# Kernel optimization log

Measured on AMD Instinct MI355X. Metric: run time of the kernel, lower is better.

Reference implementation:

```python
import jax, jax.numpy as jnp
import numpy as np

N_QUBITS = 8
DEPTH = 1
INPUT_DIM = 64
HIDDEN = 8  # must equal N_QUBITS
SEQ = 64
BATCH = 256


def _apply_rx(state, wire, ang):
    # state: (B, 2, 2, ..., 2) with wire w on axis 1+w; ang: (B,) angles
    n = state.ndim - 1
    st = jnp.moveaxis(state, 1 + wire, -1)
    a0, a1 = st[..., 0], st[..., 1]
    half = ang * 0.5
    c = jnp.cos(half).reshape((-1,) + (1,) * (n - 1))
    s = jnp.sin(half).reshape((-1,) + (1,) * (n - 1))
    new = jnp.stack([c * a0 - 1j * s * a1, c * a1 - 1j * s * a0], axis=-1)
    return jnp.moveaxis(new, -1, 1 + wire)


def _apply_cnot(state, cw, tw):
    st = jnp.moveaxis(state, (1 + cw, 1 + tw), (-2, -1))
    st = st.at[..., 1, :].set(st[..., 1, ::-1])  # flip target where control=1
    return jnp.moveaxis(st, (-2, -1), (1 + cw, 1 + tw))


def qgate(theta, qparams):
    # theta: (B, n) data-dependent RX angles; qparams: (n,) trainable RX angles
    B, n = theta.shape
    state = jnp.zeros((B,) + (2,) * n, dtype=jnp.complex64)
    state = state.at[(slice(None),) + (0,) * n].set(1.0 + 0.0j)  # |0...0>
    for w in range(n):
        state = _apply_rx(state, w, theta[:, w])
    for w in range(n - 1):
        state = _apply_cnot(state, w, w + 1)
    for w in range(n):
        state = _apply_rx(state, w, jnp.broadcast_to(qparams[w], (B,)))
    probs = jnp.abs(state) ** 2  # (B, 2, ..., 2)
    expz = []
    for w in range(n):
        pw = probs.sum(axis=tuple(a for a in range(1, n + 1) if a != 1 + w))  # (B, 2)
        expz.append(pw[:, 0] - pw[:, 1])  # <Z_w>
    return jnp.stack(expz, axis=1)  # (B, n)


def setup_inputs() -> dict:
    key = jax.random.key(0)
    ks = jax.random.split(key, 13)
    d_in = INPUT_DIM + HIDDEN
    d_out = N_QUBITS * DEPTH
    sc = 1.0 / np.sqrt(d_in)
    inp = {"inputs": jax.random.normal(ks[0], (SEQ, BATCH, INPUT_DIM), dtype=jnp.float32)}
    names = ["f", "i", "g", "o"]
    for j, nm in enumerate(names):
        inp["W" + nm] = jax.random.uniform(ks[1 + 3 * j], (d_out, d_in), minval=-sc, maxval=sc, dtype=jnp.float32)
        inp["b" + nm] = jax.random.uniform(ks[2 + 3 * j], (d_out,), minval=-sc, maxval=sc, dtype=jnp.float32)
        inp["q" + nm] = jax.random.normal(ks[3 + 3 * j], (d_out,), dtype=jnp.float32)
    return inp


def reference(inputs, Wf, bf, qf, Wi, bi, qi, Wg, bg, qg, Wo, bo, qo):
    B = inputs.shape[1]
    hx0 = jnp.zeros((B, HIDDEN), dtype=inputs.dtype)
    cx0 = jnp.zeros((B, HIDDEN), dtype=inputs.dtype)

    def step(carry, x_t):
        hx, cx = carry
        comb = jnp.concatenate([x_t, hx], axis=1)  # (B, input+hidden)
        f = jax.nn.sigmoid(qgate(comb @ Wf.T + bf, qf))
        i_ = jax.nn.sigmoid(qgate(comb @ Wi.T + bi, qi))
        g = jnp.tanh(qgate(comb @ Wg.T + bg, qg))
        o = jax.nn.sigmoid(qgate(comb @ Wo.T + bo, qo))
        cx = f * cx + i_ * g
        hx = o * jnp.tanh(cx)
        return (hx, cx), hx

    (hx, cx), outputs = jax.lax.scan(step, (hx0, cx0), inputs)
    return outputs, (hx, cx)
```

## Files before the change

### kernel.cpp

```cpp
#include <hip/hip_runtime.h>
#include <hip/hip_bf16.h>

__device__ float g_pre_static[8 * 1024 * 1024];

__device__ __forceinline__ float rcp_(float x)   { return __builtin_amdgcn_rcpf(x); }
__device__ __forceinline__ float sigm_f(float x) { return rcp_(1.0f + __expf(-x)); }
__device__ __forceinline__ float tanh_f(float x) { return 1.0f - 2.0f*rcp_(__expf(2.0f*x) + 1.0f); }
__device__ __forceinline__ float sigm(float x)  { return 1.0f/(1.0f + __expf(-x)); }
__device__ __forceinline__ float tanh_(float x) { float e = __expf(2.0f*x); return (e-1.0f)/(e+1.0f); }

template<int CTRL>
__device__ __forceinline__ float dppf(float x) {
    return __int_as_float(__builtin_amdgcn_update_dpp(
        0, __float_as_int(x), CTRL, 0xF, 0xF, true));
}

template<int IDD>
__global__ __launch_bounds__(256) void k_pre8(
    const float* __restrict__ x_,
    const float* __restrict__ W0, const float* __restrict__ b0p,
    const float* __restrict__ W1, const float* __restrict__ b1p,
    const float* __restrict__ W2, const float* __restrict__ b2p,
    const float* __restrict__ W3, const float* __restrict__ b3p,
    float* __restrict__ pre, int S, int B)
{
    constexpr int DIN = IDD + 8;
    __shared__ float xs[8][IDD];
    const int t   = blockIdx.x;
    const int tid = threadIdx.x;
    const int bl  = tid >> 5;
    const int l   = tid & 31;
    const int gp  = l >> 4, w = (l >> 1) & 7, e = l & 1;
    const int g   = 2*gp + e;
    const long b0 = (long)blockIdx.y * 8;
    const float* Wp[4] = {W0, W1, W2, W3};
    const float* bp[4] = {b0p, b1p, b2p, b3p};

    if (tid < 8*(IDD/4)) {
        int r = tid / (IDD/4), k4 = tid % (IDD/4);
        long bb = b0 + r; if (bb >= B) bb = B - 1;
        float4 v = ((const float4*)(x_ + ((long)t*B + bb)*IDD))[k4];
        ((float4*)&xs[r][0])[k4] = v;
    }

    float wr[IDD];
    {
        const float4* wv = (const float4*)(Wp[g] + (long)w*DIN);
        #pragma unroll
        for (int k4 = 0; k4 < IDD/4; ++k4) {
            float4 v = wv[k4];
            wr[4*k4] = v.x; wr[4*k4+1] = v.y; wr[4*k4+2] = v.z; wr[4*k4+3] = v.w;
        }
    }
    float a = bp[g][w];
    __syncthreads();

    const long b = b0 + bl;
    if (b >= B) return;
    const float4* xv = (const float4*)&xs[bl][0];
    #pragma unroll
    for (int k4 = 0; k4 < IDD/4; ++k4) {
        float4 v = xv[k4];
        a += wr[4*k4]*v.x + wr[4*k4+1]*v.y + wr[4*k4+2]*v.z + wr[4*k4+3]*v.w;
    }
    pre[((long)t*B + b)*32 + l] = a;
}

__global__ __launch_bounds__(256) void k_pre_gen(
    const float* __restrict__ x_,
    const float* W0, const float* b0p,
    const float* W1, const float* b1p,
    const float* W2, const float* b2p,
    const float* W3, const float* b3p,
    float* __restrict__ pre,
    int S, int B, int ID, int H, int SP)
{
    extern __shared__ float lds[];
    const int dIn  = ID + H;
    const int dInP = dIn + 1;
    float* xs    = lds;
    float* wsh   = lds + 64*SP;
    float* sbias = wsh + 4*H*dInP;
    const int t   = blockIdx.x;
    const int tid = threadIdx.x;
    const int bl  = tid & 63;
    const int q   = tid >> 6;
    const int b0  = blockIdx.y * 64;
    const float* Wp[4] = {W0, W1, W2, W3};
    const float* bp[4] = {b0p, b1p, b2p, b3p};

    for (int g = 0; g < 4; ++g)
        for (int idx = tid; idx < H*dIn; idx += 256) {
            int w = idx / dIn, k = idx - w*dIn;
            wsh[(g*H + w)*dInP + k] = Wp[g][idx];
        }
    for (int idx = tid; idx < 4*H; idx += 256)
        sbias[idx] = bp[idx / H][idx % H];

    {
        int total = 64 * ID;
        for (int i = tid; i < total; i += 256) {
            int r = i / ID, c = i - r*ID;
            long bb = (long)b0 + r; if (bb >= B) bb = B - 1;
            xs[r*SP + c] = x_[((long)t*B + bb)*ID + c];
        }
    }
    __syncthreads();

    const int b = b0 + bl;
    if (b < B) {
        const float* xrow = &xs[bl*SP];
        float* orow = pre + (((long)t*B + b)*4 + q)*H;
        for (int w = 0; w < H; ++w) {
            float acc = sbias[q*H + w];
            const float* wrow = &wsh[(q*H + w)*dInP];
            for (int k = 0; k < ID; ++k) acc += xrow[k] * wrow[k];
            orow[w] = acc;
        }
    }
}

__global__ __launch_bounds__(64) void k_rec8(
    const float* __restrict__ W0, const float* __restrict__ q0,
    const float* __restrict__ W1, const float* __restrict__ q1,
    const float* __restrict__ W2, const float* __restrict__ q2,
    const float* __restrict__ W3, const float* __restrict__ q3,
    const float* __restrict__ pre,
    float* __restrict__ out, int S, int B, int ID)
{
    const int dIn  = ID + 8;
    const int lane = threadIdx.x;
    const int w    = lane & 7;
    const int gp   = (lane >> 3) & 1;
    const int b    = blockIdx.x*4 + (lane >> 4);
    const int bs   = (b < B) ? b : (B - 1);
    const float* Wp[4] = {W0, W1, W2, W3};
    const float* qp[4] = {q0, q1, q2, q3};
    const int g0 = 2*gp, g1 = 2*gp + 1;

    float wrot0[8], wrot1[8];
    #pragma unroll
    for (int k = 0; k < 8; ++k) {
        int j = (w - k) & 7;
        wrot0[k] = Wp[g0][(long)w*dIn + ID + j];
        wrot1[k] = Wp[g1][(long)w*dIn + ID + j];
    }
    const float qv0 = qp[g0][w], qv1 = qp[g1][w];
    const float mult0 = (w < 7) ? __cosf(qv0) : 1.0f;
    const float mult1 = (w < 7) ? __cosf(qv1) : 1.0f;
    const float qadd0 = (w == 7) ? qv0 : 0.0f;
    const float qadd1 = (w == 7) ? qv1 : 0.0f;
    const float ascl = gp ? 2.0f : 1.0f;
    const float aoff = gp ? -1.0f : 0.0f;

    float cxw = 0.0f, hxw = 0.0f;
    float hxr[8];
    #pragma unroll
    for (int k = 0; k < 8; ++k) hxr[k] = 0.0f;

    const float2* base = (const float2*)(pre + (long)bs*32 + gp*16 + 2*w);
    const long tstep = (long)B*16;

    float2 pf[4];
    #pragma unroll
    for (int d = 0; d < 4; ++d) {
        int tt = (d < S) ? d : (S - 1);
        pf[d] = base[(long)tt*tstep];
    }

    for (int t0 = 0; t0 < S; t0 += 4) {
        #pragma unroll
        for (int d = 0; d < 4; ++d) {
            const int t = t0 + d;
            if (t < S) {
                float2 pc = pf[d];
                int tn = t + 4; if (tn >= S) tn = S - 1;
                pf[d] = base[(long)tn*tstep];

                float th0 = pc.x, th1 = pc.y;
                #pragma unroll
                for (int k = 0; k < 8; ++k) {
                    th0 = fmaf(wrot0[k], hxr[k], th0);
                    th1 = fmaf(wrot1[k], hxr[k], th1);
                }
                float P0 = __cosf(th0 + qadd0);
                float P1 = __cosf(th1 + qadd1);

                float s;
                s = dppf<0x111>(P0); P0 *= (w >= 1) ? s : 1.0f;
                s = dppf<0x111>(P1); P1 *= (w >= 1) ? s : 1.0f;
                s = dppf<0x112>(P0); P0 *= (w >= 2) ? s : 1.0f;
                s = dppf<0x112>(P1); P1 *= (w >= 2) ? s : 1.0f;
                s = dppf<0x114>(P0); P0 *= (w >= 4) ? s : 1.0f;
                s = dppf<0x114>(P1); P1 *= (w >= 4) ? s : 1.0f;

                float act0 = ascl * sigm_f(ascl * (mult0 * P0)) + aoff;
                float act1 = sigm_f(mult1 * P1);

                float ex0 = dppf<0x128>(act0);
                float ex1 = dppf<0x128>(act1);
                float fv = gp ? ex0  : act0;
                float iv = gp ? ex1  : act1;
                float gv = gp ? act0 : ex0;
                float ov = gp ? act1 : ex1;

                cxw = fv*cxw + iv*gv;
                hxw = ov * tanh_f(cxw);

                if (gp == 0 && b < B) out[((long)t*B + b)*8 + w] = hxw;

                hxr[0] = hxw;
                hxr[1] = dppf<0x121>(hxw);
                hxr[2] = dppf<0x122>(hxw);
                hxr[3] = dppf<0x123>(hxw);
                hxr[4] = dppf<0x124>(hxw);
                hxr[5] = dppf<0x125>(hxw);
                hxr[6] = dppf<0x126>(hxw);
                hxr[7] = dppf<0x127>(hxw);
            }
        }
    }

    if (gp == 0 && b < B) {
        out[((long)S*B + b)*8 + w]     = hxw;
        out[((long)S*B + B + b)*8 + w] = cxw;
    }
}

__global__ __launch_bounds__(64) void k_rec_g(
    const float* __restrict__ pre,
    const float* W0, const float* q0,
    const float* W1, const float* q1,
    const float* W2, const float* q2,
    const float* W3, const float* q3,
    float* __restrict__ out, int S, int B, int ID, int H)
{
    __shared__ float sWh[4*32*32];
    __shared__ float scq[4*32];
    const int dIn = ID + H;
    const int tid = threadIdx.x;
    const int b   = blockIdx.x*64 + tid;
    const float* Wp[4] = {W0, W1, W2, W3};
    const float* qp[4] = {q0, q1, q2, q3};

    for (int idx = tid; idx < 4*H*H; idx += 64) {
        int g = idx / (H*H), r = idx % (H*H);
        int w = r / H, j = r % H;
        sWh[(g*H + w)*H + j] = Wp[g][(long)w*dIn + ID + j];
    }
    for (int idx = tid; idx < 4*H; idx += 64) {
        int g = idx / H, w = idx % H;
        float qv = qp[g][w];
        scq[idx] = (w < H-1) ? __cosf(qv) : qv;
    }
    __syncthreads();
    if (b >= B) return;

    float hx[32], cx[32], gate[4][32], th[32];
    for (int w = 0; w < H; ++w) { hx[w] = 0.0f; cx[w] = 0.0f; }

    for (int t = 0; t < S; ++t) {
        const float* pt = pre + ((long)t*B + b)*4*H;
        for (int g = 0; g < 4; ++g) {
            for (int w = 0; w < H; ++w) {
                float a = pt[g*H + w];
                const float* wrp = &sWh[(g*H + w)*H];
                for (int j = 0; j < H; ++j) a += wrp[j]*hx[j];
                th[w] = a;
            }
            float cum = 1.0f;
            for (int w = 0; w < H-1; ++w) {
                cum *= __cosf(th[w]);
                gate[g][w] = scq[g*H + w] * cum;
            }
            gate[g][H-1] = cum * __cosf(th[H-1] + scq[g*H + H-1]);
        }
        float* orow = out + ((long)t*B + b)*H;
        for (int w = 0; w < H; ++w) {
            float fv = sigm (gate[0][w]);
            float iv = sigm (gate[1][w]);
            float gv = tanh_(gate[2][w]);
            float ov = sigm (gate[3][w]);
            cx[w] = fv*cx[w] + iv*gv;
            hx[w] = ov*tanh_(cx[w]);
            orow[w] = hx[w];
        }
    }
    float* oh = out + ((long)S*B + b)*H;
    float* oc = out + ((long)S*B + B + b)*H;
    for (int w = 0; w < H; ++w) { oh[w] = hx[w]; oc[w] = cx[w]; }
}

static bool derive(long sz[13], long osz, long& S, long& B, long& ID, long& H) {
    H = sz[3];
    long dIn = (H > 0) ? sz[1] / H : 0;
    ID = dIn - H;
    long TB = (ID > 0) ? sz[0] / ID : 0;
    B = (H > 0) ? (osz / H - TB) / 2 : 0;
    S = (B > 0) ? TB / B : 0;
    return (H >= 1 && H <= 32 && ID >= 1 && B >= 1 && S >= 1 &&
            S*B == TB && (S*B + 2*B)*H == osz &&
            dIn*H == sz[1] && TB*ID == sz[0]);
}

extern "C" void kernel_launch(void* const* d_in, const int* in_sizes, int n_in,
                              void* d_out, int out_size, void* d_ws, size_t ws_size,
                              hipStream_t stream) {
    const float* x  = (const float*)d_in[0];
    const float* Wf = (const float*)d_in[1];  const float* bfv = (const float*)d_in[2];  const float* qf = (const float*)d_in[3];
    const float* Wi = (const float*)d_in[4];  const float* biv = (const float*)d_in[5];  const float* qi = (const float*)d_in[6];
    const float* Wg = (const float*)d_in[7];  const float* bgv = (const float*)d_in[8];  const float* qg = (const float*)d_in[9];
    const float* Wo = (const float*)d_in[10]; const float* bov = (const float*)d_in[11]; const float* qo = (const float*)d_in[12];
    float* out = (float*)d_out;

    long S = 0, B = 0, ID = 0, H = 0;
    bool ok = false;
    for (int scale : {1, 4, 2}) {
        long sz[13];
        for (int i = 0; i < 13; ++i) sz[i] = (long)in_sizes[i] / scale;
        long osz = (long)out_size / scale;
        if (derive(sz, osz, S, B, ID, H)) { ok = true; break; }
    }
    if (!ok) { H = 8; ID = 64; B = 256; S = 64; }
    long dIn = ID + H;

    size_t pre_bytes = (size_t)S * 4 * H * B * sizeof(float);
    float* pre = (ws_size >= pre_bytes) ? (float*)d_ws : g_pre_static;

    if (H == 8 && ID == 64) {
        k_pre8<64><<<dim3((unsigned)S, (unsigned)((B + 7) / 8)), dim3(256), 0, stream>>>(
            x, Wf, bfv, Wi, biv, Wg, bgv, Wo, bov, pre, (int)S, (int)B);
        k_rec8<<<dim3((unsigned)((B + 3) / 4)), dim3(64), 0, stream>>>(
            Wf, qf, Wi, qi, Wg, qg, Wo, qo, pre, out, (int)S, (int)B, (int)ID);
    } else {
        int SP = (int)ID + 1;
        size_t lds_bytes = (size_t)(64*SP + 4*H*(dIn + 1) + 4*H) * sizeof(float);
        k_pre_gen<<<dim3((unsigned)S, (unsigned)((B + 63) / 64)), dim3(256), lds_bytes, stream>>>(
            x, Wf, bfv, Wi, biv, Wg, bgv, Wo, bov, pre,
            (int)S, (int)B, (int)ID, (int)H, SP);
        k_rec_g<<<dim3((unsigned)((B + 63) / 64)), dim3(64), 0, stream>>>(
            pre, Wf, qf, Wi, qi, Wg, qg, Wo, qo, out, (int)S, (int)B, (int)ID, (int)H);
    }
}
```

Before: 104.0 us.

## Fuse input projection and recurrence into one kernel with LDS-staged preactivations

For the default shape (H=8, ID=64, S<=64), a single kernel now computes the input-side gate preactivations for four batch rows across all timesteps into shared memory. One wavefront of the block then runs the recurrent quantum-LSTM loop reading from LDS. This removes the second kernel launch and the global-memory round trip of the preactivation buffer. The cost is that the projection phase uses only 64 blocks of 512 threads, and most threads sit idle during the serial recurrence.

```diff
diff --git a/kernel.cpp b/kernel.cpp
--- a/kernel.cpp
+++ b/kernel.cpp
@@ -13,6 +13,170 @@
 __device__ __forceinline__ float dppf(float x) {
     return __int_as_float(__builtin_amdgcn_update_dpp(
         0, __float_as_int(x), CTRL, 0xF, 0xF, true));
+}
+
+template<int IDD>
+__global__ __launch_bounds__(512) void k_fused8(
+    const float* __restrict__ x_,
+    const float* __restrict__ W0, const float* __restrict__ b0p, const float* __restrict__ q0v,
+    const float* __restrict__ W1, const float* __restrict__ b1p, const float* __restrict__ q1v,
+    const float* __restrict__ W2, const float* __restrict__ b2p, const float* __restrict__ q2v,
+    const float* __restrict__ W3, const float* __restrict__ b3p, const float* __restrict__ q3v,
+    float* __restrict__ out, int S, int B)
+{
+    constexpr int DIN  = IDD + 8;
+    constexpr int SMAX = 64;
+    constexpr int TCH  = 32;
+    __shared__ float xs[4][TCH][IDD];
+    __shared__ float ps[SMAX][4][32];
+
+    const int tid = threadIdx.x;
+    const long b0 = (long)blockIdx.x * 4;
+    const float* Wp[4] = {W0, W1, W2, W3};
+    const float* bp[4] = {b0p, b1p, b2p, b3p};
+    const float* qp[4] = {q0v, q1v, q2v, q3v};
+
+    const int l  = tid & 31;
+    const int b4 = (tid >> 5) & 3;
+    const int hh = tid >> 7;
+    const int gp = l >> 4, w8 = (l >> 1) & 7, e = l & 1;
+    const int g  = 2*gp + e;
+
+    float wr[IDD];
+    {
+        const float4* wv = (const float4*)(Wp[g] + (long)w8*DIN);
+        #pragma unroll
+        for (int k4 = 0; k4 < IDD/4; ++k4) {
+            float4 v = wv[k4];
+            wr[4*k4] = v.x; wr[4*k4+1] = v.y; wr[4*k4+2] = v.z; wr[4*k4+3] = v.w;
+        }
+    }
+    const float bias = bp[g][w8];
+
+    for (int c = 0; c < S; c += TCH) {
+        {
+            const int nf4 = 4 * TCH * (IDD/4);
+            for (int idx = tid; idx < nf4; idx += 512) {
+                int k4 = idx & (IDD/4 - 1);
+                int r  = idx >> 4;
+                int bs = r >> 5;
+                int tl = r & (TCH - 1);
+                int t  = c + tl; if (t >= S) t = S - 1;
+                long bb = b0 + bs; if (bb >= B) bb = B - 1;
+                float4 v = ((const float4*)(x_ + ((long)t*B + bb)*IDD))[k4];
+                ((float4*)&xs[bs][tl][0])[k4] = v;
+            }
+        }
+        __syncthreads();
+        #pragma unroll
+        for (int i = 0; i < TCH/4; ++i) {
+            int t = c + hh*(TCH/4) + i;
+            if (t < S) {
+                const float4* xv = (const float4*)&xs[b4][t - c][0];
+                float a0 = bias, a1 = 0.0f, a2 = 0.0f, a3 = 0.0f;
+                #pragma unroll
+                for (int k4 = 0; k4 < IDD/4; ++k4) {
+                    float4 v = xv[k4];
+                    a0 = fmaf(wr[4*k4],   v.x, a0);
+                    a1 = fmaf(wr[4*k4+1], v.y, a1);
+                    a2 = fmaf(wr[4*k4+2], v.z, a2);
+                    a3 = fmaf(wr[4*k4+3], v.w, a3);
+                }
+                ps[t][b4][l] = (a0 + a1) + (a2 + a3);
+            }
+        }
+        __syncthreads();
+    }
+
+    if (tid >= 64) return;
+
+    const int lane = tid;
+    const int w    = lane & 7;
+    const int gpr  = (lane >> 3) & 1;
+    const long b   = b0 + (lane >> 4);
+    const int g0 = 2*gpr, g1 = 2*gpr + 1;
+
+    float wrot0[8], wrot1[8];
+    #pragma unroll
+    for (int k = 0; k < 8; ++k) {
+        int j = (w - k) & 7;
+        wrot0[k] = Wp[g0][(long)w*DIN + IDD + j];
+        wrot1[k] = Wp[g1][(long)w*DIN + IDD + j];
+    }
+    const float qv0 = qp[g0][w], qv1 = qp[g1][w];
+    const float mult0 = (w < 7) ? __cosf(qv0) : 1.0f;
+    const float mult1 = (w < 7) ? __cosf(qv1) : 1.0f;
+    const float qadd0 = (w == 7) ? qv0 : 0.0f;
+    const float qadd1 = (w == 7) ? qv1 : 0.0f;
+    const float ascl = gpr ? 2.0f : 1.0f;
+    const float aoff = gpr ? -1.0f : 0.0f;
+
+    float cxw = 0.0f, hxw = 0.0f;
+    float hxr[8];
+    #pragma unroll
+    for (int k = 0; k < 8; ++k) hxr[k] = 0.0f;
+
+    const float2* pbase = (const float2*)(&ps[0][lane >> 4][gpr*16 + 2*w]);
+
+    float2 pn = pbase[0];
+    #pragma unroll 2
+    for (int t = 0; t < S; ++t) {
+        float2 pc = pn;
+        int tn = (t + 1 < S) ? (t + 1) : (S - 1);
+        pn = pbase[(long)tn * 64];
+
+        float tA0 = pc.x, tA1 = pc.y, tB0, tB1;
+        tA0 = fmaf(wrot0[0], hxr[0], tA0);  tA1 = fmaf(wrot1[0], hxr[0], tA1);
+        tA0 = fmaf(wrot0[1], hxr[1], tA0);  tA1 = fmaf(wrot1[1], hxr[1], tA1);
+        tA0 = fmaf(wrot0[2], hxr[2], tA0);  tA1 = fmaf(wrot1[2], hxr[2], tA1);
+        tA0 = fmaf(wrot0[3], hxr[3], tA0);  tA1 = fmaf(wrot1[3], hxr[3], tA1);
+        tB0 = wrot0[4]*hxr[4];              tB1 = wrot1[4]*hxr[4];
+        tB0 = fmaf(wrot0[5], hxr[5], tB0);  tB1 = fmaf(wrot1[5], hxr[5], tB1);
+        tB0 = fmaf(wrot0[6], hxr[6], tB0);  tB1 = fmaf(wrot1[6], hxr[6], tB1);
+        tB0 = fmaf(wrot0[7], hxr[7], tB0);  tB1 = fmaf(wrot1[7], hxr[7], tB1);
+        float th0 = tA0 + tB0;
+        float th1 = tA1 + tB1;
+
+        float P0 = __cosf(th0 + qadd0);
+        float P1 = __cosf(th1 + qadd1);
+
+        float s;
+        s = dppf<0x111>(P0); P0 *= (w >= 1) ? s : 1.0f;
+        s = dppf<0x111>(P1); P1 *= (w >= 1) ? s : 1.0f;
+        s = dppf<0x112>(P0); P0 *= (w >= 2) ? s : 1.0f;
+        s = dppf<0x112>(P1); P1 *= (w >= 2) ? s : 1.0f;
+        s = dppf<0x114>(P0); P0 *= (w >= 4) ? s : 1.0f;
+        s = dppf<0x114>(P1); P1 *= (w >= 4) ? s : 1.0f;
+
+        float act0 = ascl * sigm_f(ascl * (mult0 * P0)) + aoff;
+        float act1 = sigm_f(mult1 * P1);
+
+        float ex0 = dppf<0x128>(act0);
+        float ex1 = dppf<0x128>(act1);
+        float fv = gpr ? ex0  : act0;
+        float iv = gpr ? ex1  : act1;
+        float gv = gpr ? act0 : ex0;
+        float ov = gpr ? act1 : ex1;
+
+        cxw = fv*cxw + iv*gv;
+        hxw = ov * tanh_f(cxw);
+
+        if (gpr == 0 && b < B) out[((long)t*B + b)*8 + w] = hxw;
+
+        hxr[0] = hxw;
+        hxr[1] = dppf<0x121>(hxw);
+        hxr[2] = dppf<0x122>(hxw);
+        hxr[3] = dppf<0x123>(hxw);
+        hxr[4] = dppf<0x124>(hxw);
+        hxr[5] = dppf<0x125>(hxw);
+        hxr[6] = dppf<0x126>(hxw);
+        hxr[7] = dppf<0x127>(hxw);
+    }
+
+    if (gpr == 0 && b < B) {
+        out[((long)S*B + b)*8 + w]     = hxw;
+        out[((long)S*B + B + b)*8 + w] = cxw;
+    }
 }
 
 template<int IDD>
@@ -324,6 +488,13 @@
     if (!ok) { H = 8; ID = 64; B = 256; S = 64; }
     long dIn = ID + H;
 
+    if (H == 8 && ID == 64 && S <= 64) {
+        k_fused8<64><<<dim3((unsigned)((B + 3) / 4)), dim3(512), 0, stream>>>(
+            x, Wf, bfv, qf, Wi, biv, qi, Wg, bgv, qg, Wo, bov, qo,
+            out, (int)S, (int)B);
+        return;
+    }
+
     size_t pre_bytes = (size_t)S * 4 * H * B * sizeof(float);
     float* pre = (ws_size >= pre_bytes) ? (float*)d_ws : g_pre_static;
 
```

After: 102.8 us. Within noise of the previous version (-1.1%).
